# Kernel optimization log

Measured on AMD Instinct MI355X. Metric: run time of the kernel, lower is better.

Reference implementation:

```python
import jax, jax.numpy as jnp
import numpy as np

B, K, BIN = 16, 2048, 256
GRU, EMB, HID = 1024, 1024, 1024
H, KV = 16, 4
D = HID // H          # 64 head dim
NREP = H // KV        # 4 GQA repeat factor


def rotate_half(x):
    x1, x2 = jnp.split(x, 2, axis=-1)
    return jnp.concatenate((-x2, x1), axis=-1)


def setup_inputs() -> dict:
    key = jax.random.key(0)
    ks = jax.random.split(key, 8)
    h = jax.random.normal(ks[0], (B, K, GRU), dtype=jnp.float32)
    # real RoPE frequency tables, shape (BIN, D)
    inv_freq = 1.0 / (10000.0 ** (jnp.arange(0, D, 2, dtype=jnp.float32) / D))
    t = jnp.arange(BIN, dtype=jnp.float32)
    freqs = jnp.outer(t, inv_freq)                      # (BIN, D/2)
    emb = jnp.concatenate((freqs, freqs), axis=-1)      # (BIN, D)
    freqs_cos, freqs_sin = jnp.cos(emb), jnp.sin(emb)
    s = lambda fan: 1.0 / np.sqrt(fan).astype(np.float32)
    Wq = jax.random.normal(ks[1], (H * D, EMB), jnp.float32) * s(EMB)
    Wk = jax.random.normal(ks[2], (KV * D, GRU), jnp.float32) * s(GRU)
    Wv = jax.random.normal(ks[3], (KV * D, GRU), jnp.float32) * s(GRU)
    Wo = jax.random.normal(ks[4], (EMB, H * D), jnp.float32) * s(H * D)
    output_queries = jax.random.normal(ks[5], (BIN, EMB), jnp.float32)
    Wr = jax.random.normal(ks[6], (2, EMB), jnp.float32) * s(EMB)
    br = jnp.zeros((2,), jnp.float32)
    return {"h": h, "freqs_cos": freqs_cos, "freqs_sin": freqs_sin,
            "Wq": Wq, "Wk": Wk, "Wv": Wv, "Wo": Wo,
            "output_queries": output_queries, "Wr": Wr, "br": br}


def reference(h, freqs_cos, freqs_sin, Wq, Wk, Wv, Wo, output_queries, Wr, br):
    # KV projections from GRU history: (B, K, KV, D)
    k = (h @ Wk.T).reshape(B, K, KV, D)
    v = (h @ Wv.T).reshape(B, K, KV, D)
    # Queries are batch-invariant learned tokens: (BIN, H, D)
    q = (output_queries @ Wq.T).reshape(BIN, H, D)
    cos = freqs_cos[:, None, :]  # (BIN, 1, D) broadcast over heads
    sin = freqs_sin[:, None, :]
    q = q * cos + rotate_half(q) * sin
    # GQA: repeat_interleave KV heads to H heads
    k_rep = jnp.repeat(k, NREP, axis=2)  # (B, K, H, D)
    v_rep = jnp.repeat(v, NREP, axis=2)
    scores = jnp.einsum('qhd,bkhd->bhqk', q, k_rep) / np.sqrt(D).astype(np.float32)
    attn = jax.nn.softmax(scores, axis=-1)               # dropout p=0 (eval)
    out = jnp.einsum('bhqk,bkhd->bqhd', attn, v_rep).reshape(B, BIN, H * D)
    z = out @ Wo.T                                        # (B, BIN, EMB)
    return z @ Wr.T + br                                  # (B, BIN, 2)
```

## Files before the change

kernel.cpp:

```cpp
#include <hip/hip_runtime.h>

typedef __attribute__((ext_vector_type(8))) short short8;
typedef __attribute__((ext_vector_type(4))) float f32x4;
typedef __attribute__((ext_vector_type(16))) float f32x16;

#define DEV static __device__ __forceinline__

DEV unsigned short f2bf(float f) {
  unsigned int u = __float_as_uint(f);
  u += 0x7fff + ((u >> 16) & 1);
  return (unsigned short)(u >> 16);
}

DEV unsigned int cvtpk(float lo, float hi) {
  unsigned int r;
  asm("v_cvt_pk_bf16_f32 %0, %1, %2" : "=v"(r) : "v"(lo), "v"(hi));
  return r;
}

DEV f32x4 mfma16(short8 a, short8 b, f32x4 c) {
  return __builtin_amdgcn_mfma_f32_16x16x32_bf16(a, b, c, 0, 0, 0);
}

DEV f32x16 mfma32(short8 a, short8 b, f32x16 c) {
  return __builtin_amdgcn_mfma_f32_32x32x16_bf16(a, b, c, 0, 0, 0);
}

DEV void gl_lds16(const void* g, void* l) {
  __builtin_amdgcn_global_load_lds((const __attribute__((address_space(1))) void*)g,
                                   (__attribute__((address_space(3))) void*)l, 16, 0, 0);
}

__global__ __launch_bounds__(256) void cvtB_kernel(const float* __restrict__ Wq,
                                                   const float* __restrict__ Wk,
                                                   const float* __restrict__ Wv,
                                                   unsigned short* __restrict__ wqb,
                                                   unsigned short* __restrict__ wkvb) {
  int id = blockIdx.x * 256 + threadIdx.x;
  int e = id * 4;
  float4 v;
  unsigned short* d;
  if (e < 1048576)      { v = *(const float4*)(Wq + e);             d = wqb + e; }
  else if (e < 1310720) { v = *(const float4*)(Wk + (e - 1048576)); d = wkvb + (e - 1048576); }
  else                  { v = *(const float4*)(Wv + (e - 1310720)); d = wkvb + 262144 + (e - 1310720); }
  uint2 pk;
  pk.x = cvtpk(v.x, v.y);
  pk.y = cvtpk(v.z, v.w);
  *(uint2*)d = pk;
}

__global__ __launch_bounds__(256) void wrp_partial(const float* __restrict__ Wr,
                                                   const float* __restrict__ Wo,
                                                   float* __restrict__ part) {
  int blk = blockIdx.x;
  int tid = threadIdx.x;
  float a0[4] = {0.f,0.f,0.f,0.f};
  float a1[4] = {0.f,0.f,0.f,0.f};
  int e0 = blk * 64;
  for (int e = e0; e < e0 + 64; e++) {
    float w0 = Wr[e];
    float w1 = Wr[1024 + e];
    #pragma unroll
    for (int j4 = 0; j4 < 4; j4++) {
      float wo = Wo[(size_t)e * 1024 + j4 * 256 + tid];
      a0[j4] += w0 * wo;
      a1[j4] += w1 * wo;
    }
  }
  #pragma unroll
  for (int j4 = 0; j4 < 4; j4++) {
    part[blk * 2048 + 0    + j4 * 256 + tid] = a0[j4];
    part[blk * 2048 + 1024 + j4 * 256 + tid] = a1[j4];
  }
}

__global__ __launch_bounds__(256) void wrp_reduce(const float* __restrict__ part,
                                                  float* __restrict__ Wrp) {
  int id = blockIdx.x * 256 + threadIdx.x;
  float s = 0.f;
  #pragma unroll
  for (int blk = 0; blk < 16; blk++) s += part[blk * 2048 + id];
  Wrp[id] = s;
}

__global__ __launch_bounds__(512, 4) void gemm_kv(const float* __restrict__ A,
                                                  const unsigned short* __restrict__ Bb,
                                                  unsigned short* __restrict__ ok,
                                                  unsigned short* __restrict__ ov) {
  __shared__ unsigned short Asl[2][2048];
  __shared__ unsigned short Bsl[2][16384];

  int bid = blockIdx.x;
  int m0 = bid * 64;

  int tid = threadIdx.x;
  int w = tid >> 6, l = tid & 63;
  int l4 = l >> 4, l15 = l & 15;
  int wm = w >> 2, wn = w & 3;

  int arow = tid >> 3;
  const float* ga = A + (size_t)(m0 + arow) * 1024 + (tid & 7) * 4;
  int awb = arow * 64 + (tid & 7) * 8;

  const unsigned short* gb = Bb + (size_t)(tid >> 2) * 1024 + (tid & 3) * 8;
  int bdst = tid * 16;

  int aoff = (wm * 32 + l15) * 64 + l4 * 16;
  int boff = (wn * 128 + l15) * 64 + l4 * 16;

  f32x4 acc[2][8];
  #pragma unroll
  for (int i = 0; i < 2; i++)
    #pragma unroll
    for (int j = 0; j < 8; j++) acc[i][j] = (f32x4)(0.f);

  #define STAGEB(bufi, tt)                                                  \
    { const unsigned short* s0 = gb + (tt) * 32;                            \
      char* d0 = (char*)Bsl[bufi] + bdst;                                   \
      gl_lds16(s0,          d0);                                            \
      gl_lds16(s0 + 131072, d0 + 8192);                                     \
      gl_lds16(s0 + 262144, d0 + 16384);                                    \
      gl_lds16(s0 + 393216, d0 + 24576); }

  #define WRITEA(bufi, av)                                                  \
    { uint2 pk2;                                                            \
      pk2.x = cvtpk(av.x, av.y);                                            \
      pk2.y = cvtpk(av.z, av.w);                                            \
      *(uint2*)((char*)Asl[bufi] + awb) = pk2; }

  {
    float4 a0 = *(const float4*)(ga);
    STAGEB(0, 0);
    WRITEA(0, a0);
  }
  __syncthreads();

  for (int t = 0; t < 32; t++) {
    int buf = t & 1;
    float4 an;
    if (t + 1 < 32) {
      STAGEB(buf ^ 1, t + 1);
      an = *(const float4*)(ga + (t + 1) * 32);
    }

    short8 af[2];
    #pragma unroll
    for (int i = 0; i < 2; i++)
      af[i] = *(const short8*)((char*)Asl[buf] + aoff + i * 1024);
    #pragma unroll
    for (int j = 0; j < 8; j++) {
      short8 bf = *(const short8*)((char*)Bsl[buf] + boff + j * 1024);
      #pragma unroll
      for (int i = 0; i < 2; i++)
        acc[i][j] = mfma16(af[i], bf, acc[i][j]);
    }

    if (t + 1 < 32) WRITEA(buf ^ 1, an);
    __syncthreads();
  }
  #undef STAGEB
  #undef WRITEA

  #pragma unroll
  for (int i = 0; i < 2; i++)
    #pragma unroll
    for (int j = 0; j < 8; j++) {
      int n = wn * 128 + j * 16 + l15;
      int kvv = n >> 6, d = n & 63;
      #pragma unroll
      for (int r = 0; r < 4; r++) {
        int m = m0 + wm * 32 + i * 16 + l4 * 4 + r;
        int bb = m >> 11, kk = m & 2047;
        unsigned short val = f2bf(acc[i][j][r]);
        if (kvv < 4)
          ok[((size_t)(bb * 4 + kvv) * 2048 + kk) * 64 + d] = val;
        else
          ov[((size_t)(bb * 4 + (kvv - 4)) * 64 + d) * 2048 + kk] = val;
      }
    }
}

__global__ __launch_bounds__(256) void gemm_q(const float* __restrict__ A,
                                              const unsigned short* __restrict__ Bb,
                                              float* __restrict__ of) {
  __shared__ unsigned short Asm[2][4096];
  __shared__ unsigned short Bsm[2][4096];

  int bid = blockIdx.x;
  int ksplit = bid >> 4;
  int m0 = ((bid >> 3) & 1) * 128;
  int n0 = (bid & 7) * 128;
  int t0 = ksplit * 8;
  constexpr int nt = 8;

  int tid = threadIdx.x;
  int w = tid >> 6, l = tid & 63;
  int l4 = l >> 4, l15 = l & 15;
  int wm = w >> 1, wn = w & 1;

  int ra = w * 32 + (l >> 1);
  int rx = (l >> 2) & 3;
  const float* ga = A + (size_t)(m0 + ra) * 1024 + t0 * 32 + (l & 1) * 16;
  int pw0 = (2 * (l & 1) + 0) ^ rx;
  int pw1 = (2 * (l & 1) + 1) ^ rx;
  int awb0 = ra * 64 + pw0 * 16;
  int awb1 = ra * 64 + pw1 * 16;

  int rb = w * 32 + (l >> 2);
  int cb = ((l & 3) ^ ((l >> 3) & 3)) * 8;
  const unsigned short* gb = Bb + (size_t)(n0 + rb) * 1024 + t0 * 32 + cb;

  int qsw = l4 ^ ((l15 >> 1) & 3);
  int arb = (wm * 64 + l15) * 64 + qsw * 16;
  int brb = (wn * 64 + l15) * 64 + qsw * 16;

  f32x4 acc[4][4];
  #pragma unroll
  for (int i = 0; i < 4; i++)
    #pragma unroll
    for (int j = 0; j < 4; j++) acc[i][j] = (f32x4)(0.f);

  float4 fa0, fa1, fa2, fa3;

  #define LOADA(tt)                                                        \
    { const float* gA = ga + (tt) * 32;                                    \
      fa0 = *(const float4*)(gA);                                          \
      fa1 = *(const float4*)(gA + 4);                                      \
      fa2 = *(const float4*)(gA + 8);                                      \
      fa3 = *(const float4*)(gA + 12); }

  #define WRITEA(bufi)                                                     \
    { union { short8 s; unsigned int u[4]; } t0u, t1u;                     \
      t0u.u[0] = cvtpk(fa0.x, fa0.y); t0u.u[1] = cvtpk(fa0.z, fa0.w);      \
      t0u.u[2] = cvtpk(fa1.x, fa1.y); t0u.u[3] = cvtpk(fa1.z, fa1.w);      \
      t1u.u[0] = cvtpk(fa2.x, fa2.y); t1u.u[1] = cvtpk(fa2.z, fa2.w);      \
      t1u.u[2] = cvtpk(fa3.x, fa3.y); t1u.u[3] = cvtpk(fa3.z, fa3.w);      \
      *(short8*)((char*)Asm[bufi] + awb0) = t0u.s;                         \
      *(short8*)((char*)Asm[bufi] + awb1) = t1u.s; }

  #define STAGEB(bufi, tt)                                                 \
    { char* lb = (char*)Bsm[bufi] + w * 2048;                              \
      const unsigned short* gB = gb + (tt) * 32;                           \
      gl_lds16(gB, lb);                                                    \
      gl_lds16(gB + 16384, lb + 1024); }

  LOADA(0);
  STAGEB(0, 0);
  WRITEA(0);
  __syncthreads();

  for (int t = 0; t < nt; t++) {
    int buf = t & 1;
    if (t + 1 < nt) {
      LOADA(t + 1);
      STAGEB(buf ^ 1, t + 1);
    }
    short8 af[4], bfg[4];
    #pragma unroll
    for (int i = 0; i < 4; i++)
      af[i] = *(const short8*)((char*)Asm[buf] + arb + i * 1024);
    #pragma unroll
    for (int j = 0; j < 4; j++)
      bfg[j] = *(const short8*)((char*)Bsm[buf] + brb + j * 1024);
    #pragma unroll
    for (int i = 0; i < 4; i++)
      #pragma unroll
      for (int j = 0; j < 4; j++)
        acc[i][j] = mfma16(af[i], bfg[j], acc[i][j]);
    if (t + 1 < nt) WRITEA(buf ^ 1);
    __syncthreads();
  }
  #undef LOADA
  #undef WRITEA
  #undef STAGEB

  float* o = of + (size_t)ksplit * 262144;
  #pragma unroll
  for (int i = 0; i < 4; i++)
    #pragma unroll
    for (int j = 0; j < 4; j++) {
      int n = n0 + wn * 64 + j * 16 + l15;
      #pragma unroll
      for (int r = 0; r < 4; r++) {
        int m = m0 + wm * 64 + i * 16 + l4 * 4 + r;
        o[(size_t)m * 1024 + n] = acc[i][j][r];
      }
    }
}

__global__ __launch_bounds__(256) void rope_kernel(const float* __restrict__ qp,
                                                   const float* __restrict__ cosb,
                                                   const float* __restrict__ sinb,
                                                   unsigned short* __restrict__ qb) {
  int id = blockIdx.x * 256 + threadIdx.x;
  int qrow = id >> 10, hd = id & 1023, hh = hd >> 6, d = hd & 63;
  int od = hh * 64 + ((d < 32) ? d + 32 : d - 32);
  float v = 0.f, o = 0.f;
  #pragma unroll
  for (int s4 = 0; s4 < 4; s4++) {
    v += qp[s4 * 262144 + qrow * 1024 + hd];
    o += qp[s4 * 262144 + qrow * 1024 + od];
  }
  if (d < 32) o = -o;
  float c = cosb[qrow * 64 + d];
  float s = sinb[qrow * 64 + d];
  float outv = (v * c + o * s) * 0.18033688011112042f;
  qb[((size_t)hh * 256 + qrow) * 64 + d] = f2bf(outv);
}

__global__ __launch_bounds__(256) void attn_kernel(const unsigned short* __restrict__ qb,
                                                   const unsigned short* __restrict__ kb,
                                                   const unsigned short* __restrict__ vb,
                                                   const float* __restrict__ Wrp,
                                                   float* __restrict__ part) {
  __shared__ unsigned short Kt[2][2048];
  __shared__ unsigned short Vt[2][2048];


  int bid = blockIdx.x;
  int x = bid & 7, mid = (bid >> 3) & 7, top = bid >> 6;
  int g = mid * 8 + x;
  int b = g >> 2, kvh = g & 3;
  int hl = top >> 1, qh = top & 1;
  int h = kvh * 4 + hl;

  int tid = threadIdx.x;
  int w = tid >> 6, l = tid & 63;
  int q31 = l & 31, L = l >> 5;
  int qg = qh * 128 + w * 32 + q31;

  const unsigned short* kg = kb + (size_t)(b * 4 + kvh) * 2048 * 64;
  const unsigned short* vg = vb + (size_t)(b * 4 + kvh) * 64 * 2048;

  short8 qf[4];
  #pragma unroll
  for (int c = 0; c < 4; c++)
    qf[c] = *(const short8*)&qb[((size_t)h * 256 + qg) * 64 + c * 16 + L * 8];

  f32x16 Ot[2];
  Ot[0] = (f32x16)(0.f); Ot[1] = (f32x16)(0.f);
  float m = -1e30f, lsum = 0.f;

  int ksrow = tid >> 3, kslot = tid & 7;
  const unsigned short* ksrc = kg + (size_t)ksrow * 64 + ((kslot ^ (ksrow & 7)) * 8);
  int vsrow = tid >> 2, vslot = tid & 3;
  const unsigned short* vsrc = vg + (size_t)vsrow * 2048 + ((vslot ^ (vsrow & 3)) * 8);

  #define STAGE(bufi, tt)                                                    \
    { gl_lds16(ksrc + (size_t)(tt) * 2048, (char*)Kt[bufi] + tid * 16);      \
      gl_lds16(vsrc + (tt) * 32,           (char*)Vt[bufi] + tid * 16); }

  STAGE(0, 0);
  __syncthreads();

  for (int t = 0; t < 64; t++) {
    int buf = t & 1;
    if (t + 1 < 64) STAGE(buf ^ 1, t + 1);

    f32x16 st = (f32x16)(0.f);
    #pragma unroll
    for (int c = 0; c < 4; c++) {
      int row = q31;
      int byt = row * 128 + (((c * 2 + L) ^ (row & 7)) * 16);
      short8 kf = *(const short8*)((char*)Kt[buf] + byt);
      st = mfma32(kf, qf[c], st);
    }

    float mx = fmaxf(fmaxf(fmaxf(st[0], st[1]), fmaxf(st[2], st[3])),
                     fmaxf(fmaxf(st[4], st[5]), fmaxf(st[6], st[7])));
    float mx2 = fmaxf(fmaxf(fmaxf(st[8], st[9]), fmaxf(st[10], st[11])),
                      fmaxf(fmaxf(st[12], st[13]), fmaxf(st[14], st[15])));
    mx = fmaxf(mx, mx2);
    mx = fmaxf(mx, __shfl_xor(mx, 32));

    if (!__all(mx <= m + 8.f)) {
      float mnew = fmaxf(m, mx);
      float corr = exp2f(m - mnew);
      lsum *= corr;
      #pragma unroll
      for (int db = 0; db < 2; db++)
        #pragma unroll
        for (int r = 0; r < 16; r++) Ot[db][r] *= corr;
      m = mnew;
    }

    float p[16];
    float ls = 0.f;
    #pragma unroll
    for (int r = 0; r < 16; r++) {
      p[r] = exp2f(st[r] - m);
      ls += p[r];
    }
    lsum += ls;

    unsigned int pw[2][4];
    #pragma unroll
    for (int kc = 0; kc < 2; kc++) {
      unsigned int A0 = cvtpk(p[kc * 8 + 0], p[kc * 8 + 1]);
      unsigned int A1 = cvtpk(p[kc * 8 + 2], p[kc * 8 + 3]);
      unsigned int B0 = cvtpk(p[kc * 8 + 4], p[kc * 8 + 5]);
      unsigned int B1 = cvtpk(p[kc * 8 + 6], p[kc * 8 + 7]);
      asm volatile("v_permlane32_swap_b32 %0, %1" : "+v"(A0), "+v"(B0));
      asm volatile("v_permlane32_swap_b32 %0, %1" : "+v"(A1), "+v"(B1));
      pw[kc][0] = A0; pw[kc][1] = A1; pw[kc][2] = B0; pw[kc][3] = B1;
    }

    #pragma unroll
    for (int db = 0; db < 2; db++) {
      int drow = db * 32 + q31;
      #pragma unroll
      for (int kc = 0; kc < 2; kc++) {
        int byt = drow * 64 + (((kc * 2 + L) ^ (drow & 3)) * 16);
        short8 vf = *(const short8*)((char*)Vt[buf] + byt);
        short8 pf;
        {
          union { short8 s; unsigned int u[4]; } uu;
          uu.u[0] = pw[kc][0]; uu.u[1] = pw[kc][1];
          uu.u[2] = pw[kc][2]; uu.u[3] = pw[kc][3];
          pf = uu.s;
        }
        Ot[db] = mfma32(vf, pf, Ot[db]);
      }
    }

    __syncthreads();
  }
  #undef STAGE

  lsum += __shfl_xor(lsum, 32);
  float rinv = 1.0f / lsum;

  float a0 = 0.f, a1 = 0.f;
  #pragma unroll
  for (int db = 0; db < 2; db++)
    #pragma unroll
    for (int rq = 0; rq < 4; rq++) {
      int dbase = db * 32 + rq * 8 + L * 4;
      float4 w0v = *(const float4*)(Wrp + h * 64 + dbase);
      float4 w1v = *(const float4*)(Wrp + 1024 + h * 64 + dbase);
      #pragma unroll
      for (int j = 0; j < 4; j++) {
        float o = Ot[db][rq * 4 + j] * rinv;
        a0 += o * ((const float*)&w0v)[j];
        a1 += o * ((const float*)&w1v)[j];
      }
    }
  a0 += __shfl_xor(a0, 32);
  a1 += __shfl_xor(a1, 32);

  if (L == 0) {
    size_t base = ((size_t)(b * 16 + h) * 256 + qg) * 2;
    float2 r2; r2.x = a0; r2.y = a1;
    *(float2*)&part[base] = r2;
  }
}

__global__ __launch_bounds__(256) void final_kernel(const float* __restrict__ part,
                                                    const float* __restrict__ br,
                                                    float* __restrict__ out) {
  int id = blockIdx.x * 256 + threadIdx.x;
  int c = id & 1, q = (id >> 1) & 255, b = id >> 9;
  float s = br[c];
  #pragma unroll
  for (int hh = 0; hh < 16; hh++)
    s += part[(((size_t)(b * 16 + hh) * 256) + q) * 2 + c];
  out[id] = s;
}

extern "C" void kernel_launch(void* const* d_in, const int* in_sizes, int n_in,
                              void* d_out, int out_size, void* d_ws, size_t ws_size,
                              hipStream_t stream) {
  const float* h    = (const float*)d_in[0];
  const float* fcos = (const float*)d_in[1];
  const float* fsin = (const float*)d_in[2];
  const float* Wq   = (const float*)d_in[3];
  const float* Wk   = (const float*)d_in[4];
  const float* Wv   = (const float*)d_in[5];
  const float* Wo   = (const float*)d_in[6];
  const float* oq   = (const float*)d_in[7];
  const float* Wr   = (const float*)d_in[8];
  const float* br   = (const float*)d_in[9];
  float* out = (float*)d_out;

  char* ws = (char*)d_ws;
  unsigned short* kbuf = (unsigned short*)(ws);
  unsigned short* vbuf = (unsigned short*)(ws + 16777216);
  float* qpart         = (float*)(ws + 33554432);
  unsigned short* qbf  = (unsigned short*)(ws + 37748736);
  float* wpart         = (float*)(ws + 38273024);
  float* Wrp           = (float*)(ws + 38404096);
  float* apart         = (float*)(ws + 38412288);
  unsigned short* wqb  = (unsigned short*)(ws + 38936576);
  unsigned short* wkvb = (unsigned short*)(ws + 41033728);

  cvtB_kernel<<<dim3(1536), dim3(256), 0, stream>>>(Wq, Wk, Wv, wqb, wkvb);
  wrp_partial<<<dim3(16), dim3(256), 0, stream>>>(Wr, Wo, wpart);
  wrp_reduce<<<dim3(8), dim3(256), 0, stream>>>(wpart, Wrp);
  gemm_q<<<dim3(64), dim3(256), 0, stream>>>(oq, wqb, qpart);
  rope_kernel<<<dim3(1024), dim3(256), 0, stream>>>(qpart, fcos, fsin, qbf);
  gemm_kv<<<dim3(512), dim3(512), 0, stream>>>(h, wkvb, kbuf, vbuf);
  attn_kernel<<<dim3(512), dim3(256), 0, stream>>>(qbf, kbuf, vbuf, Wrp, apart);
  final_kernel<<<dim3(32), dim3(256), 0, stream>>>(apart, br, out);
}
```

Measured before the change: 174.3 us.

## Load KV-GEMM A operand directly into registers, swizzle B LDS, remap blocks

The KV projection GEMM stops staging the fp32 activation tile through LDS. Each wave now reads its A fragments straight from global memory, converts them to bf16 in registers and feeds them to MFMA. The warp tiling changes so every wave covers all 64 rows and a 64-column slice. An XOR swizzle is added to the B LDS layout to avoid bank conflicts, and block indices are remapped for better L2 locality. The cost is that all 8 waves now read the same A rows redundantly from global/L2, and those loads are no longer prefetched a stage ahead.

Result: slower. 270.6 us (+55.3%).

```diff
diff --git a/kernel.cpp b/kernel.cpp
--- a/kernel.cpp
+++ b/kernel.cpp
@@ -87,32 +87,29 @@
                                                   const unsigned short* __restrict__ Bb,
                                                   unsigned short* __restrict__ ok,
                                                   unsigned short* __restrict__ ov) {
-  __shared__ unsigned short Asl[2][2048];
   __shared__ unsigned short Bsl[2][16384];
 
   int bid = blockIdx.x;
-  int m0 = bid * 64;
+  int sw = (bid & 7) * 64 + (bid >> 3);
+  int m0 = sw * 64;
 
   int tid = threadIdx.x;
   int w = tid >> 6, l = tid & 63;
   int l4 = l >> 4, l15 = l & 15;
-  int wm = w >> 2, wn = w & 3;
-
-  int arow = tid >> 3;
-  const float* ga = A + (size_t)(m0 + arow) * 1024 + (tid & 7) * 4;
-  int awb = arow * 64 + (tid & 7) * 8;
-
-  const unsigned short* gb = Bb + (size_t)(tid >> 2) * 1024 + (tid & 3) * 8;
+
+  const unsigned short* gb = Bb + (size_t)(tid >> 2) * 1024
+                                + ((tid & 3) ^ ((tid >> 3) & 3)) * 8;
   int bdst = tid * 16;
 
-  int aoff = (wm * 32 + l15) * 64 + l4 * 16;
-  int boff = (wn * 128 + l15) * 64 + l4 * 16;
-
-  f32x4 acc[2][8];
-  #pragma unroll
-  for (int i = 0; i < 2; i++)
-    #pragma unroll
-    for (int j = 0; j < 8; j++) acc[i][j] = (f32x4)(0.f);
+  const float* ga = A + (size_t)(m0 + l15) * 1024 + l4 * 8;
+
+  int boff = (w * 64 + l15) * 64 + ((l4 ^ ((l15 >> 1) & 3)) * 16);
+
+  f32x4 acc[4][4];
+  #pragma unroll
+  for (int i = 0; i < 4; i++)
+    #pragma unroll
+    for (int j = 0; j < 4; j++) acc[i][j] = (f32x4)(0.f);
 
   #define STAGEB(bufi, tt)                                                  \
     { const unsigned short* s0 = gb + (tt) * 32;                            \
@@ -122,54 +119,43 @@
       gl_lds16(s0 + 262144, d0 + 16384);                                    \
       gl_lds16(s0 + 393216, d0 + 24576); }
 
-  #define WRITEA(bufi, av)                                                  \
-    { uint2 pk2;                                                            \
-      pk2.x = cvtpk(av.x, av.y);                                            \
-      pk2.y = cvtpk(av.z, av.w);                                            \
-      *(uint2*)((char*)Asl[bufi] + awb) = pk2; }
-
-  {
-    float4 a0 = *(const float4*)(ga);
-    STAGEB(0, 0);
-    WRITEA(0, a0);
-  }
+  STAGEB(0, 0);
   __syncthreads();
 
   for (int t = 0; t < 32; t++) {
     int buf = t & 1;
-    float4 an;
-    if (t + 1 < 32) {
-      STAGEB(buf ^ 1, t + 1);
-      an = *(const float4*)(ga + (t + 1) * 32);
-    }
-
-    short8 af[2];
-    #pragma unroll
-    for (int i = 0; i < 2; i++)
-      af[i] = *(const short8*)((char*)Asl[buf] + aoff + i * 1024);
-    #pragma unroll
-    for (int j = 0; j < 8; j++) {
-      short8 bf = *(const short8*)((char*)Bsl[buf] + boff + j * 1024);
-      #pragma unroll
-      for (int i = 0; i < 2; i++)
-        acc[i][j] = mfma16(af[i], bf, acc[i][j]);
-    }
-
-    if (t + 1 < 32) WRITEA(buf ^ 1, an);
+    if (t + 1 < 32) STAGEB(buf ^ 1, t + 1);
+
+    short8 bf[4];
+    #pragma unroll
+    for (int j = 0; j < 4; j++)
+      bf[j] = *(const short8*)((char*)Bsl[buf] + boff + j * 1024);
+
+    #pragma unroll
+    for (int i = 0; i < 4; i++) {
+      const float* gA = ga + i * 16384 + t * 32;
+      float4 x = *(const float4*)(gA);
+      float4 y = *(const float4*)(gA + 4);
+      union { short8 s; unsigned int u[4]; } af;
+      af.u[0] = cvtpk(x.x, x.y); af.u[1] = cvtpk(x.z, x.w);
+      af.u[2] = cvtpk(y.x, y.y); af.u[3] = cvtpk(y.z, y.w);
+      #pragma unroll
+      for (int j = 0; j < 4; j++)
+        acc[i][j] = mfma16(af.s, bf[j], acc[i][j]);
+    }
     __syncthreads();
   }
   #undef STAGEB
-  #undef WRITEA
-
-  #pragma unroll
-  for (int i = 0; i < 2; i++)
-    #pragma unroll
-    for (int j = 0; j < 8; j++) {
-      int n = wn * 128 + j * 16 + l15;
+
+  #pragma unroll
+  for (int i = 0; i < 4; i++)
+    #pragma unroll
+    for (int j = 0; j < 4; j++) {
+      int n = w * 64 + j * 16 + l15;
       int kvv = n >> 6, d = n & 63;
       #pragma unroll
       for (int r = 0; r < 4; r++) {
-        int m = m0 + wm * 32 + i * 16 + l4 * 4 + r;
+        int m = m0 + i * 16 + l4 * 4 + r;
         int bb = m >> 11, kk = m & 2047;
         unsigned short val = f2bf(acc[i][j][r]);
         if (kvv < 4)
@@ -315,7 +301,6 @@
                                                    float* __restrict__ part) {
   __shared__ unsigned short Kt[2][2048];
   __shared__ unsigned short Vt[2][2048];
-
 
   int bid = blockIdx.x;
   int x = bid & 7, mid = (bid >> 3) & 7, top = bid >> 6;
```
